# Optimization experiments

Hardware: AMD Instinct MI355X
Metric: run time of the kernel (lower is better)

## Reference

```python
import jax, jax.numpy as jnp
import numpy as np
from jax import lax

HEADS = 8
WIN_SIZES = (2, 4, 8)


def _linear(x, w, b):
    return x @ w + b


def _window_attention(x2d, ws, w4, b4):
    # x2d: (B,H,W,C); w4: (4,C,C) = [q,k,v,out]; b4: (4,C)
    B, H, W, C = x2d.shape
    p1, p2 = H // ws, W // ws
    xw = x2d.reshape(B, p1, ws, p2, ws, C).transpose(0, 1, 3, 2, 4, 5)
    xw = xw.reshape(B, p1, p2, ws * ws, C)
    hs = C // HEADS
    q = _linear(xw, w4[0], b4[0]).reshape(B, p1, p2, ws * ws, HEADS, hs)
    k = _linear(xw, w4[1], b4[1]).reshape(B, p1, p2, ws * ws, HEADS, hs)
    v = _linear(xw, w4[2], b4[2]).reshape(B, p1, p2, ws * ws, HEADS, hs)
    scores = jnp.einsum('bpqwhd,bpqvhd->bpqhwv', q, k) / jnp.sqrt(jnp.asarray(hs, x2d.dtype))
    probs = jax.nn.softmax(scores, axis=-1)
    ctx = jnp.einsum('bpqhwv,bpqvhd->bpqwhd', probs, v).reshape(B, p1, p2, ws * ws, C)
    return _linear(ctx, w4[3], b4[3])


def _unwindow(out, ws):
    B, p1, p2, win, C = out.shape
    s = out.reshape(B, p1, p2, ws, ws, C).transpose(0, 1, 3, 2, 4, 5)
    return s.reshape(B, p1 * ws, p2 * ws, C)


def _up_bilinear_ac(x, oh, ow):
    # x: (B,C,h,w); bilinear with align_corners=True (UpsamplingBilinear2d)
    B, C, h, w = x.shape
    def grid(o, i):
        pos = jnp.arange(o, dtype=x.dtype) * ((i - 1) / (o - 1))
        i0 = jnp.floor(pos).astype(jnp.int32)
        i1 = jnp.minimum(i0 + 1, i - 1)
        return i0, i1, pos - i0.astype(x.dtype)
    r0, r1, tr = grid(oh, h)
    c0, c1, tc = grid(ow, w)
    xr = x[:, :, r0, :] * (1 - tr)[None, None, :, None] + x[:, :, r1, :] * tr[None, None, :, None]
    return xr[:, :, :, c0] * (1 - tc) + xr[:, :, :, c1] * tc


def _forward(x, attn_w, attn_b, edge_w, mlp_w1, mlp_b1, mlp_w2, mlp_b2,
             dl_w, dl_b, ax_w, ax_b, g_shift, g_bias, sq_w, sq_b):
    B, N, C = x.shape
    H = W = int(np.sqrt(N))
    x2d = x.reshape(B, H, W, C)

    # multi-scale window attention branches
    scale_outputs = [_unwindow(_window_attention(x2d, ws, attn_w[i], attn_b[i]), ws)
                     for i, ws in enumerate(WIN_SIZES)]

    # adaptive window selector
    xc = x2d.transpose(0, 3, 1, 2)  # (B,C,H,W)
    edge = jnp.abs(lax.conv_general_dilated(xc, edge_w, (1, 1), 'SAME'))
    avg = lax.reduce_window(edge, 0.0, lax.add, (1, 1, 3, 3), (1, 1, 1, 1), 'SAME') / 9.0
    e = avg.transpose(0, 2, 3, 1)  # (B,H,W,1)
    wts = jax.nn.softmax(jax.nn.relu(e @ mlp_w1 + mlp_b1) @ mlp_w2 + mlp_b2, axis=-1)

    blended = sum(wts[..., i:i + 1] * scale_outputs[i] for i in range(len(WIN_SIZES)))
    h_map = blended.transpose(0, 3, 1, 2)  # (B,C,H,W)

    # ws=4 window attention -> DlightConv token pooling
    x_win = _window_attention(x2d, 4, attn_w[1], attn_b[1])  # (B,p,p,16,C)
    probs = jax.nn.softmax(jnp.mean(x_win, axis=-2) @ dl_w + dl_b, axis=-1)
    x_dl = jnp.sum(x_win * probs[..., None], axis=-2)  # (B,p,p,C)

    # axial attention (no head split, no scaling in the axial branch)
    q = _linear(x_dl, ax_w[0], ax_b[0])
    k = _linear(x_dl, ax_w[1], ax_b[1])
    v = _linear(x_dl, ax_w[2], ax_b[2])
    scores_x = jnp.einsum('bhwc,bhvc->bhwv', q, k)  # (B,r,c,k)
    scores_y = jnp.einsum('bhwc,bvwc->bwhv', q, k)  # (B,c,r,k)

    # GaussianTrans: vectorized per-pixel gaussian positional bias
    p = x_dl.shape[1]
    idx = jnp.arange(p, dtype=x.dtype)
    dist2 = (idx[None, :] - idx[:, None]) ** 2          # [pos, k]
    gb = -(g_shift[0] * dist2 + g_bias[0])              # (p,p)
    ax = jax.nn.softmax(scores_x + gb[None, None, :, :], axis=-1)       # bias indexed by c
    ay = jax.nn.softmax(jnp.swapaxes(scores_y, 1, 2) + gb[None, :, None, :], axis=-1)  # bias by r
    x_g = jnp.einsum('brck,brkd->brcd', ax, v) + jnp.einsum('brck,bkcd->brcd', ay, v)

    x_g = _up_bilinear_ac(x_g.transpose(0, 3, 1, 2), H, W)  # (B,C,H,W)

    cat = jnp.concatenate([x_g, h_map], axis=1)  # (B,2C,H,W)
    out = jnp.einsum('oc,bchw->bohw', sq_w, cat) + sq_b[None, :, None, None]
    return out.transpose(0, 2, 3, 1).reshape(B, N, C)


def setup_inputs() -> dict:
    key = jax.random.key(0)
    ks = jax.random.split(key, 16)
    B, N, C = 16, 4096, 256
    s = 0.02
    return {
        'x': jax.random.normal(ks[0], (B, N, C), jnp.float32),
        'attn_w': jax.random.normal(ks[1], (3, 4, C, C), jnp.float32) * s,
        'attn_b': jax.random.normal(ks[2], (3, 4, C), jnp.float32) * s,
        'edge_w': jax.random.normal(ks[3], (1, C, 3, 3), jnp.float32) * s,
        'mlp_w1': jax.random.normal(ks[4], (1, 16), jnp.float32) * s,
        'mlp_b1': jax.random.normal(ks[5], (16,), jnp.float32) * s,
        'mlp_w2': jax.random.normal(ks[6], (16, 3), jnp.float32) * s,
        'mlp_b2': jax.random.normal(ks[7], (3,), jnp.float32) * s,
        'dl_w': jax.random.normal(ks[8], (C, 16), jnp.float32) * s,
        'dl_b': jax.random.normal(ks[9], (16,), jnp.float32) * s,
        'ax_w': jax.random.normal(ks[10], (3, C, C), jnp.float32) * s,
        'ax_b': jax.random.normal(ks[11], (3, C), jnp.float32) * s,
        'g_shift': jnp.abs(jax.random.normal(ks[12], (1,), jnp.float32)),
        'g_bias': -jnp.abs(jax.random.normal(ks[13], (1,), jnp.float32)),
        'sq_w': jax.random.normal(ks[14], (C, 2 * C), jnp.float32) * s,
        'sq_b': jax.random.normal(ks[15], (C,), jnp.float32) * s,
    }


def reference(x, attn_w, attn_b, edge_w, mlp_w1, mlp_b1, mlp_w2, mlp_b2,
              dl_w, dl_b, ax_w, ax_b, g_shift, g_bias, sq_w, sq_b):
    return _forward(x, attn_w, attn_b, edge_w, mlp_w1, mlp_b1, mlp_w2, mlp_b2,
                    dl_w, dl_b, ax_w, ax_b, g_shift, g_bias, sq_w, sq_b)
```

## Files before the change

kernel.cpp:

```cpp
#include <hip/hip_runtime.h>
#include <math.h>


#define CHUNK_B 4
#define CHUNK_TOK (CHUNK_B * 4096)
#define KS 32

typedef __attribute__((ext_vector_type(8))) short short8;
typedef __attribute__((ext_vector_type(8))) unsigned short ushort8;
typedef __attribute__((ext_vector_type(4))) float f32x4;

__device__ __forceinline__ ushort f2bf(float f) {
    union { float f; unsigned u; } v; v.f = f;
    unsigned r = v.u + 0x7fff + ((v.u >> 16) & 1);
    return (ushort)(r >> 16);
}
__device__ __forceinline__ float bf2f(ushort h) {
    union { unsigned u; float f; } v; v.u = ((unsigned)h) << 16; return v.f;
}
__device__ __forceinline__ void split2(float v, ushort& h, ushort& l) {
    h = f2bf(v);
    l = f2bf(v - bf2f(h));
}

__device__ __forceinline__ void gld16(const ushort* g, ushort* l) {
    __builtin_amdgcn_global_load_lds(
        (const __attribute__((address_space(1))) unsigned int*)g,
        (__attribute__((address_space(3))) unsigned int*)l,
        16, 0, 0);
}

__global__ __launch_bounds__(256) void split_w_kmajor(
    const float* __restrict__ W, ushort* __restrict__ Th, ushort* __restrict__ Tl, int nmats)
{
    const int idx = blockIdx.x * 256 + threadIdx.x;
    if (idx >= nmats * 65536) return;
    const int mat = idx >> 16, r = idx & 65535;
    const int n = r >> 8, k = r & 255;
    const float v = W[(size_t)mat * 65536 + k * 256 + n];
    ushort h, l; split2(v, h, l);
    Th[idx] = h; Tl[idx] = l;
}
__global__ __launch_bounds__(256) void split_w_nmajor(
    const float* __restrict__ W, ushort* __restrict__ Th, ushort* __restrict__ Tl, int total)
{
    const int idx = blockIdx.x * 256 + threadIdx.x;
    if (idx >= total) return;
    ushort h, l; split2(W[idx], h, l);
    Th[idx] = h; Tl[idx] = l;
}

#define GEMM_DECLS                                                            \
    __shared__ ushort Ah[128 * KS], Al[128 * KS], Bh[128 * KS], Bl[128 * KS]; \
    const int tid = threadIdx.x;                                              \
    const int wave = tid >> 6, lane = tid & 63;                               \
    const int quad = lane >> 4, l16 = lane & 15;                              \
    const int wr = (wave >> 1) * 64, wc = (wave & 1) * 64;                    \
    f32x4 acc[4][4];                                                          \
    _Pragma("unroll") for (int i = 0; i < 4; i++)                             \
        _Pragma("unroll") for (int j = 0; j < 4; j++)                         \
            acc[i][j] = (f32x4){0.f, 0.f, 0.f, 0.f};                          \
    const int srow = tid >> 1;                                    \
    const int skp  = (tid & 1) * 16;

#define STAGE_GLD(dstbuf, srcp, strideE, rowbase, k0e)                        \
    _Pragma("unroll") for (int jj = 0; jj < 2; jj++) {                        \
        const int rr = (wave << 5) + (jj << 4) + (lane >> 2);                 \
        gld16((srcp) + (size_t)((rowbase) + rr) * (strideE) + (k0e) + ((lane & 3) << 3), \
              (dstbuf) + (wave << 10) + (jj << 9));                           \
    }

#define STAGE_A_SPLIT(Aptr, kk)                                               \
    {                                                                         \
        const float* srcp = (Aptr) + (size_t)(m0 + srow) * 256 + (kk) + skp;  \
        _Pragma("unroll") for (int c = 0; c < 2; c++) {                       \
            float4 v0 = *(const float4*)(srcp + c * 8);                       \
            float4 v1 = *(const float4*)(srcp + c * 8 + 4);                   \
            ushort8 h, l; ushort hh, ll;                                      \
            split2(v0.x, hh, ll); h[0] = hh; l[0] = ll;                       \
            split2(v0.y, hh, ll); h[1] = hh; l[1] = ll;                       \
            split2(v0.z, hh, ll); h[2] = hh; l[2] = ll;                       \
            split2(v0.w, hh, ll); h[3] = hh; l[3] = ll;                       \
            split2(v1.x, hh, ll); h[4] = hh; l[4] = ll;                       \
            split2(v1.y, hh, ll); h[5] = hh; l[5] = ll;                       \
            split2(v1.z, hh, ll); h[6] = hh; l[6] = ll;                       \
            split2(v1.w, hh, ll); h[7] = hh; l[7] = ll;                       \
            *(ushort8*)&Ah[srow * KS + skp + c * 8] = h;                      \
            *(ushort8*)&Al[srow * KS + skp + c * 8] = l;                      \
        }                                                                     \
    }

#define GEMM_COMPUTE                                                          \
    {                                                                         \
        short8 afh[4], afl[4], bfh[4], bfl[4];                                \
        _Pragma("unroll") for (int i = 0; i < 4; i++) {                       \
            const int ro = (wr + i * 16 + l16) * KS + quad * 8;               \
            afh[i] = *(const short8*)&Ah[ro];                                 \
            afl[i] = *(const short8*)&Al[ro];                                 \
        }                                                                     \
        _Pragma("unroll") for (int j = 0; j < 4; j++) {                       \
            const int no = (wc + j * 16 + l16) * KS + quad * 8;               \
            bfh[j] = *(const short8*)&Bh[no];                                 \
            bfl[j] = *(const short8*)&Bl[no];                                 \
        }                                                                     \
        _Pragma("unroll") for (int i = 0; i < 4; i++)                         \
            _Pragma("unroll") for (int j = 0; j < 4; j++) {                   \
                acc[i][j] = __builtin_amdgcn_mfma_f32_16x16x32_bf16(          \
                    afh[i], bfh[j], acc[i][j], 0, 0, 0);                      \
                acc[i][j] = __builtin_amdgcn_mfma_f32_16x16x32_bf16(          \
                    afl[i], bfh[j], acc[i][j], 0, 0, 0);                      \
                acc[i][j] = __builtin_amdgcn_mfma_f32_16x16x32_bf16(          \
                    afh[i], bfl[j], acc[i][j], 0, 0, 0);                      \
            }                                                                 \
    }

__global__ __launch_bounds__(256, 2) void gemm3_mfma(
    const float* __restrict__ A,
    const ushort* __restrict__ Wth, const ushort* __restrict__ Wtl,
    const float* __restrict__ b0, const float* __restrict__ b1, const float* __restrict__ b2,
    float* __restrict__ O0, float* __restrict__ O1, float* __restrict__ O2)
{
    const int m0 = blockIdx.x * 128;
    const int mat = blockIdx.y >> 1;
    const int col0 = (blockIdx.y & 1) * 128;
    const ushort* wth = Wth + (size_t)mat * 65536 + (size_t)col0 * 256;
    const ushort* wtl = Wtl + (size_t)mat * 65536 + (size_t)col0 * 256;
    GEMM_DECLS
    for (int k0 = 0; k0 < 256; k0 += 32) {
        STAGE_GLD(Bh, wth, 256, 0, k0)
        STAGE_GLD(Bl, wtl, 256, 0, k0)
        STAGE_A_SPLIT(A, k0)
        __syncthreads();
        GEMM_COMPUTE
        __syncthreads();
    }
    const float* bias = (mat == 0) ? b0 : (mat == 1) ? b1 : b2;
    float* O = (mat == 0) ? O0 : (mat == 1) ? O1 : O2;
#pragma unroll
    for (int j = 0; j < 4; j++) {
        const int col = col0 + wc + j * 16 + l16;
        const float bj = bias[col];
#pragma unroll
        for (int i = 0; i < 4; i++) {
            const int rbase = m0 + wr + i * 16 + quad * 4;
#pragma unroll
            for (int r = 0; r < 4; r++)
                O[(size_t)(rbase + r) * 256 + col] = acc[i][j][r] + bj;
        }
    }
}

__global__ __launch_bounds__(256, 2) void gemmp_mfma(
    const ushort* __restrict__ AgH, const ushort* __restrict__ AgL,
    const ushort* __restrict__ Wth, const ushort* __restrict__ Wtl,
    const float* __restrict__ bias,
    float* __restrict__ Sout, int store_s,
    float* __restrict__ Blnd, const float* __restrict__ wts, int scale_idx, int blend_init,
    int row_off)
{
    const int m0 = blockIdx.x * 128;
    const int col0 = blockIdx.y * 128;
    const ushort* wth = Wth + (size_t)col0 * 256;
    const ushort* wtl = Wtl + (size_t)col0 * 256;
    GEMM_DECLS
    (void)srow; (void)skp;
    for (int k0 = 0; k0 < 256; k0 += 32) {
        STAGE_GLD(Ah, AgH, 256, m0, k0)
        STAGE_GLD(Al, AgL, 256, m0, k0)
        STAGE_GLD(Bh, wth, 256, 0, k0)
        STAGE_GLD(Bl, wtl, 256, 0, k0)
        __syncthreads();
        GEMM_COMPUTE
        __syncthreads();
    }
#pragma unroll
    for (int i = 0; i < 4; i++) {
        const int rbase = m0 + wr + i * 16 + quad * 4;
#pragma unroll
        for (int r = 0; r < 4; r++) {
            const size_t grow = (size_t)row_off + rbase + r;
            const float wt = wts[grow * 3 + scale_idx];
#pragma unroll
            for (int j = 0; j < 4; j++) {
                const int col = col0 + wc + j * 16 + l16;
                const float v = acc[i][j][r] + bias[col];
                if (store_s) Sout[grow * 256 + col] = v;
                float* bp = Blnd + grow * 256 + col;
                if (blend_init) *bp = wt * v;
                else            *bp = *bp + wt * v;
            }
        }
    }
}

__global__ __launch_bounds__(256, 2) void gemmf_mfma(
    const ushort* __restrict__ UPH, const ushort* __restrict__ UPL,
    const float* __restrict__ BLD,
    const ushort* __restrict__ Wth, const ushort* __restrict__ Wtl,
    const float* __restrict__ SQB, float* __restrict__ OUT)
{
    const int m0 = blockIdx.x * 128;
    const int col0 = blockIdx.y * 128;
    const ushort* wth = Wth + (size_t)col0 * 512;
    const ushort* wtl = Wtl + (size_t)col0 * 512;
    GEMM_DECLS
    for (int k0 = 0; k0 < 512; k0 += 32) {
        STAGE_GLD(Bh, wth, 512, 0, k0)
        STAGE_GLD(Bl, wtl, 512, 0, k0)
        if (k0 < 256) {
            STAGE_GLD(Ah, UPH, 256, m0, k0)
            STAGE_GLD(Al, UPL, 256, m0, k0)
        } else {
            STAGE_A_SPLIT(BLD, (k0 & 255))
        }
        __syncthreads();
        GEMM_COMPUTE
        __syncthreads();
    }
#pragma unroll
    for (int j = 0; j < 4; j++) {
        const int col = col0 + wc + j * 16 + l16;
        const float bj = SQB[col];
#pragma unroll
        for (int i = 0; i < 4; i++) {
            const int rbase = m0 + wr + i * 16 + quad * 4;
#pragma unroll
            for (int r = 0; r < 4; r++)
                OUT[(size_t)(rbase + r) * 256 + col] = acc[i][j][r] + bj;
        }
    }
}

template <int WS, int NH>
__global__ __launch_bounds__(256) void win_attn(
    const float* __restrict__ Q, const float* __restrict__ K,
    const float* __restrict__ V, ushort* __restrict__ CTXh, ushort* __restrict__ CTXl)
{
    constexpr int WIN = WS * WS;
    constexpr int NW = 64 / WS;
    constexpr int CW = NH * 32;
    __shared__ float qs[WIN][CW + 4], ks[WIN][CW + 4], vs[WIN][CW + 4];
    __shared__ float sc[NH][WIN][WIN + 1];
    const int tid = threadIdx.x;
    const int wid = blockIdx.x;
    const int b = wid / (NW * NW);
    const int rem = wid % (NW * NW);
    const int p = rem / NW, q = rem % NW;
    const int h0 = blockIdx.y * NH;

    for (int idx = tid; idx < WIN * CW; idx += 256) {
        const int i = idx / CW;
        const int cc = idx % CW;
        const int ti = i / WS, tj = i % WS;
        const size_t g = ((size_t)(b * 4096 + (p * WS + ti) * 64 + (q * WS + tj))) * 256 + h0 * 32 + cc;
        qs[i][cc] = Q[g]; ks[i][cc] = K[g]; vs[i][cc] = V[g];
    }
    __syncthreads();
    const float scale = 0.17677669529663687f;
    for (int idx = tid; idx < NH * WIN * WIN; idx += 256) {
        const int hl = idx / (WIN * WIN);
        const int r = idx % (WIN * WIN);
        const int i = r / WIN, j = r % WIN;
        const int co = hl * 32;
        float s = 0.f;
#pragma unroll
        for (int d = 0; d < 32; d++) s += qs[i][co + d] * ks[j][co + d];
        sc[hl][i][j] = s * scale;
    }
    __syncthreads();
    if (tid < NH * WIN) {
        const int hl = tid / WIN, i = tid % WIN;
        float mx = -3.4e38f;
        for (int j = 0; j < WIN; j++) mx = fmaxf(mx, sc[hl][i][j]);
        float sum = 0.f;
        for (int j = 0; j < WIN; j++) {
            float e = __expf(sc[hl][i][j] - mx);
            sc[hl][i][j] = e; sum += e;
        }
        const float inv = 1.f / sum;
        for (int j = 0; j < WIN; j++) sc[hl][i][j] *= inv;
    }
    __syncthreads();
    for (int idx = tid; idx < WIN * CW; idx += 256) {
        const int i = idx / CW;
        const int cc = idx % CW;
        const int hl = cc >> 5;
        float s = 0.f;
        for (int j = 0; j < WIN; j++) s += sc[hl][i][j] * vs[j][cc];
        const int ti = i / WS, tj = i % WS;
        const size_t g = ((size_t)(b * 4096 + (p * WS + ti) * 64 + (q * WS + tj))) * 256 + h0 * 32 + cc;
        ushort hh, ll; split2(s, hh, ll);
        CTXh[g] = hh; CTXl[g] = ll;
    }
}

__global__ __launch_bounds__(256) void edge_gemm9(
    const float* __restrict__ x, const float* __restrict__ ew, float* __restrict__ ytmp)
{
    __shared__ float wsm[2304];
    const int tid = threadIdx.x;
    for (int i = tid; i < 2304; i += 256) wsm[i] = ew[i];
    __syncthreads();
    const int wave = tid >> 6, lane = tid & 63;
    const int p = blockIdx.x * 4 + wave;
    const float4 xv = *(const float4*)(x + (size_t)p * 256 + lane * 4);
    float acc[9];
#pragma unroll
    for (int t = 0; t < 9; t++) acc[t] = 0.f;
    const float xs[4] = {xv.x, xv.y, xv.z, xv.w};
#pragma unroll
    for (int i = 0; i < 4; i++) {
        const int c = lane * 4 + i;
#pragma unroll
        for (int t = 0; t < 9; t++)
            acc[t] = fmaf(xs[i], wsm[c * 9 + t], acc[t]);
    }
#pragma unroll
    for (int t = 0; t < 9; t++) {
#pragma unroll
        for (int off = 1; off < 64; off <<= 1)
            acc[t] += __shfl_xor(acc[t], off);
    }
    if (lane < 9) {
        float v = acc[0];
        switch (lane) {
            case 1: v = acc[1]; break; case 2: v = acc[2]; break;
            case 3: v = acc[3]; break; case 4: v = acc[4]; break;
            case 5: v = acc[5]; break; case 6: v = acc[6]; break;
            case 7: v = acc[7]; break; case 8: v = acc[8]; break;
            default: break;
        }
        ytmp[(size_t)p * 9 + lane] = v;
    }
}

__global__ __launch_bounds__(256) void edge_combine(
    const float* __restrict__ ytmp, float* __restrict__ edge)
{
    const int idx = blockIdx.x * 256 + threadIdx.x;
    const int b = idx >> 12, rem = idx & 4095, h = rem >> 6, w = rem & 63;
    float s = 0.f;
#pragma unroll
    for (int kh = 0; kh < 3; kh++) {
        const int hh = h + kh - 1;
        if ((unsigned)hh > 63u) continue;
#pragma unroll
        for (int kw = 0; kw < 3; kw++) {
            const int ww = w + kw - 1;
            if ((unsigned)ww > 63u) continue;
            s += ytmp[((size_t)b * 4096 + hh * 64 + ww) * 9 + kh * 3 + kw];
        }
    }
    edge[idx] = fabsf(s);
}

__global__ __launch_bounds__(256) void avg_mlp(
    const float* __restrict__ edge, const float* __restrict__ w1, const float* __restrict__ b1,
    const float* __restrict__ w2, const float* __restrict__ b2, float* __restrict__ wts)
{
    const int idx = blockIdx.x * 256 + threadIdx.x;
    const int b = idx >> 12, rem = idx & 4095, h = rem >> 6, w = rem & 63;
    float s = 0.f;
#pragma unroll
    for (int kh = -1; kh <= 1; kh++) {
        const int hh = h + kh;
        if ((unsigned)hh > 63u) continue;
#pragma unroll
        for (int kw = -1; kw <= 1; kw++) {
            const int ww = w + kw;
            if ((unsigned)ww > 63u) continue;
            s += edge[(size_t)b * 4096 + hh * 64 + ww];
        }
    }
    const float e = s / 9.f;
    float l0 = b2[0], l1 = b2[1], l2 = b2[2];
#pragma unroll
    for (int j = 0; j < 16; j++) {
        float hd = fmaxf(e * w1[j] + b1[j], 0.f);
        l0 += hd * w2[j * 3 + 0];
        l1 += hd * w2[j * 3 + 1];
        l2 += hd * w2[j * 3 + 2];
    }
    const float mx = fmaxf(l0, fmaxf(l1, l2));
    const float e0 = __expf(l0 - mx), e1 = __expf(l1 - mx), e2 = __expf(l2 - mx);
    const float inv = 1.f / (e0 + e1 + e2);
    wts[(size_t)idx * 3 + 0] = e0 * inv;
    wts[(size_t)idx * 3 + 1] = e1 * inv;
    wts[(size_t)idx * 3 + 2] = e2 * inv;
}

__global__ __launch_bounds__(256) void dlight(
    const float* __restrict__ S1, const float* __restrict__ dlw,
    const float* __restrict__ dlb, float* __restrict__ XDL)
{
    __shared__ float xw[16][257];
    __shared__ float m[256];
    __shared__ float pr[16];
    __shared__ float pr2[16];
    const int wid = blockIdx.x;
    const int b = wid >> 8, rem = wid & 255, p = rem >> 4, q = rem & 15;
    const int tid = threadIdx.x;
#pragma unroll
    for (int t = 0; t < 16; t++) {
        const int ti = t >> 2, tj = t & 3;
        xw[t][tid] = S1[((size_t)b * 4096 + (p * 4 + ti) * 64 + (q * 4 + tj)) * 256 + tid];
    }
    float mm = 0.f;
#pragma unroll
    for (int t = 0; t < 16; t++) mm += xw[t][tid];
    m[tid] = mm * (1.f / 16.f);
    __syncthreads();
    if (tid < 16) {
        float lg = dlb[tid];
        for (int c = 0; c < 256; c++) lg += m[c] * dlw[c * 16 + tid];
        pr[tid] = lg;
    }
    __syncthreads();
    if (tid < 16) {
        float mx = -3.4e38f;
        for (int j = 0; j < 16; j++) mx = fmaxf(mx, pr[j]);
        float sum = 0.f;
        for (int j = 0; j < 16; j++) sum += __expf(pr[j] - mx);
        pr2[tid] = __expf(pr[tid] - mx) / sum;
    }
    __syncthreads();
    float o = 0.f;
#pragma unroll
    for (int t = 0; t < 16; t++) o += xw[t][tid] * pr2[t];
    XDL[(size_t)wid * 256 + tid] = o;
}

__global__ __launch_bounds__(256) void axial_row(
    const float* __restrict__ Q, const float* __restrict__ K, const float* __restrict__ V,
    const float* __restrict__ gsp, const float* __restrict__ gbp, float* __restrict__ XG)
{
    __shared__ float qs[16][257], ks[16][257], vs[16][257];
    __shared__ float sc[16][17];
    const int bid = blockIdx.x;
    const int b = bid >> 4, r = bid & 15;
    const int tid = threadIdx.x;
    const float gs = gsp[0], gb = gbp[0];
#pragma unroll
    for (int w = 0; w < 16; w++) {
        const size_t base = ((size_t)b * 256 + r * 16 + w) * 256 + tid;
        qs[w][tid] = Q[base]; ks[w][tid] = K[base]; vs[w][tid] = V[base];
    }
    __syncthreads();
    {
        const int w = tid >> 4, vv = tid & 15;
        float s = 0.f;
        for (int c = 0; c < 256; c++) s += qs[w][c] * ks[vv][c];
        const float d = (float)(w - vv);
        sc[w][vv] = s - (gs * d * d + gb);
    }
    __syncthreads();
    if (tid < 16) {
        float mx = -3.4e38f;
        for (int j = 0; j < 16; j++) mx = fmaxf(mx, sc[tid][j]);
        float sum = 0.f;
        for (int j = 0; j < 16; j++) {
            float e = __expf(sc[tid][j] - mx);
            sc[tid][j] = e; sum += e;
        }
        const float inv = 1.f / sum;
        for (int j = 0; j < 16; j++) sc[tid][j] *= inv;
    }
    __syncthreads();
#pragma unroll
    for (int w2 = 0; w2 < 16; w2++) {
        float o = 0.f;
#pragma unroll
        for (int k2 = 0; k2 < 16; k2++) o += sc[w2][k2] * vs[k2][tid];
        XG[((size_t)b * 256 + r * 16 + w2) * 256 + tid] = o;
    }
}

__global__ __launch_bounds__(256) void axial_col(
    const float* __restrict__ Q, const float* __restrict__ K, const float* __restrict__ V,
    const float* __restrict__ gsp, const float* __restrict__ gbp, float* __restrict__ XG)
{
    __shared__ float qs[16][257], ks[16][257], vs[16][257];
    __shared__ float sc[16][17];
    const int bid = blockIdx.x;
    const int b = bid >> 4, col = bid & 15;
    const int tid = threadIdx.x;
    const float gs = gsp[0], gb = gbp[0];
#pragma unroll
    for (int h = 0; h < 16; h++) {
        const size_t base = ((size_t)b * 256 + h * 16 + col) * 256 + tid;
        qs[h][tid] = Q[base]; ks[h][tid] = K[base]; vs[h][tid] = V[base];
    }
    __syncthreads();
    {
        const int r = tid >> 4, vv = tid & 15;
        float s = 0.f;
        for (int c = 0; c < 256; c++) s += qs[r][c] * ks[vv][c];
        const float d = (float)(r - vv);
        sc[r][vv] = s - (gs * d * d + gb);
    }
    __syncthreads();
    if (tid < 16) {
        float mx = -3.4e38f;
        for (int j = 0; j < 16; j++) mx = fmaxf(mx, sc[tid][j]);
        float sum = 0.f;
        for (int j = 0; j < 16; j++) {
            float e = __expf(sc[tid][j] - mx);
            sc[tid][j] = e; sum += e;
        }
        const float inv = 1.f / sum;
        for (int j = 0; j < 16; j++) sc[tid][j] *= inv;
    }
    __syncthreads();
#pragma unroll
    for (int r2 = 0; r2 < 16; r2++) {
        float o = 0.f;
#pragma unroll
        for (int k2 = 0; k2 < 16; k2++) o += sc[r2][k2] * vs[k2][tid];
        XG[((size_t)b * 256 + r2 * 16 + col) * 256 + tid] += o;
    }
}

__global__ __launch_bounds__(256) void upsample(
    const float* __restrict__ XG, ushort* __restrict__ UPH, ushort* __restrict__ UPL)
{
    const unsigned idx = blockIdx.x * 256u + threadIdx.x;
    const int c = idx & 255;
    const unsigned t2 = idx >> 8;
    const int w = t2 & 63;
    const unsigned t3 = t2 >> 6;
    const int h = t3 & 63;
    const int b = t3 >> 6;
    const float rr = 15.f / 63.f;
    const float ph = h * rr, pw = w * rr;
    int h0 = (int)floorf(ph); float th = ph - (float)h0; int h1 = min(h0 + 1, 15);
    int w0 = (int)floorf(pw); float tw = pw - (float)w0; int w1 = min(w0 + 1, 15);
    const size_t bb = (size_t)b * 256;
    const float v00 = XG[((bb + h0 * 16 + w0)) * 256 + c];
    const float v10 = XG[((bb + h1 * 16 + w0)) * 256 + c];
    const float v01 = XG[((bb + h0 * 16 + w1)) * 256 + c];
    const float v11 = XG[((bb + h1 * 16 + w1)) * 256 + c];
    const float c0 = v00 * (1.f - th) + v10 * th;
    const float c1 = v01 * (1.f - th) + v11 * th;
    const float val = c0 * (1.f - tw) + c1 * tw;
    ushort hh, ll; split2(val, hh, ll);
    UPH[idx] = hh; UPL[idx] = ll;
}

extern "C" void kernel_launch(void* const* d_in, const int* in_sizes, int n_in,
                              void* d_out, int out_size, void* d_ws, size_t ws_size,
                              hipStream_t stream)
{
    const float* x      = (const float*)d_in[0];
    const float* attn_w = (const float*)d_in[1];
    const float* attn_b = (const float*)d_in[2];
    const float* edge_w = (const float*)d_in[3];
    const float* mlp_w1 = (const float*)d_in[4];
    const float* mlp_b1 = (const float*)d_in[5];
    const float* mlp_w2 = (const float*)d_in[6];
    const float* mlp_b2 = (const float*)d_in[7];
    const float* dl_w   = (const float*)d_in[8];
    const float* dl_b   = (const float*)d_in[9];
    const float* ax_w   = (const float*)d_in[10];
    const float* ax_b   = (const float*)d_in[11];
    const float* g_shift= (const float*)d_in[12];
    const float* g_bias = (const float*)d_in[13];
    const float* sq_w   = (const float*)d_in[14];
    const float* sq_b   = (const float*)d_in[15];
    float* out = (float*)d_out;

    float* ws = (float*)d_ws;
    const size_t MT = 65536;
    float* blend = ws;
    float* s1    = blend + MT * 256;
    float* scr   = s1 + MT * 256;
    float* chQ   = scr;
    float* chK   = chQ + (size_t)CHUNK_TOK * 256;
    float* chV   = chK + (size_t)CHUNK_TOK * 256;
    ushort* ctxh = (ushort*)(chV + (size_t)CHUNK_TOK * 256);
    ushort* ctxl = ctxh + (size_t)CHUNK_TOK * 256;
    ushort* uph  = (ushort*)scr;
    ushort* upl  = uph + MT * 256;
    float* ytmp  = scr;
    float* edge  = scr + MT * 256;
    float* wts   = edge + 65536;
    float* xdl   = wts + 196608;
    float* axq   = xdl + 1048576;
    float* axk   = axq + 1048576;
    float* axv   = axk + 1048576;
    float* xg    = axv + 1048576;
    ushort* Wth = (ushort*)(xg + 1048576);
    ushort* Wtl = Wth + 1114112;

    split_w_kmajor<<<(12 * 65536 + 255) / 256, 256, 0, stream>>>(attn_w, Wth, Wtl, 12);
    split_w_kmajor<<<(3 * 65536 + 255) / 256, 256, 0, stream>>>(
        ax_w, Wth + (size_t)12 * 65536, Wtl + (size_t)12 * 65536, 3);
    split_w_nmajor<<<(131072 + 255) / 256, 256, 0, stream>>>(
        sq_w, Wth + (size_t)15 * 65536, Wtl + (size_t)15 * 65536, 131072);

    edge_gemm9<<<16384, 256, 0, stream>>>(x, edge_w, ytmp);
    edge_combine<<<256, 256, 0, stream>>>(ytmp, edge);
    avg_mlp<<<256, 256, 0, stream>>>(edge, mlp_w1, mlp_b1, mlp_w2, mlp_b2, wts);

    for (int i = 0; i < 3; i++) {
        const ushort* Wh = Wth + (size_t)i * 4 * 65536;
        const ushort* Wl = Wtl + (size_t)i * 4 * 65536;
        const float* c0 = attn_b + (size_t)(i * 4 + 0) * 256;
        const float* c1 = attn_b + (size_t)(i * 4 + 1) * 256;
        const float* c2 = attn_b + (size_t)(i * 4 + 2) * 256;
        const float* c3 = attn_b + (size_t)(i * 4 + 3) * 256;
        for (int ch = 0; ch < 16 / CHUNK_B; ch++) {
            const size_t toff = (size_t)ch * CHUNK_TOK;
            const float* xc = x + toff * 256;
            gemm3_mfma<<<dim3(CHUNK_TOK / 128, 6), 256, 0, stream>>>(
                xc, Wh, Wl, c0, c1, c2, chQ, chK, chV);
            if (i == 0)
                win_attn<2, 8><<<dim3(CHUNK_B * 32 * 32, 1), 256, 0, stream>>>(chQ, chK, chV, ctxh, ctxl);
            if (i == 1)
                win_attn<4, 4><<<dim3(CHUNK_B * 16 * 16, 2), 256, 0, stream>>>(chQ, chK, chV, ctxh, ctxl);
            if (i == 2)
                win_attn<8, 1><<<dim3(CHUNK_B * 8 * 8, 8), 256, 0, stream>>>(chQ, chK, chV, ctxh, ctxl);
            gemmp_mfma<<<dim3(CHUNK_TOK / 128, 2), 256, 0, stream>>>(
                ctxh, ctxl, Wh + (size_t)3 * 65536, Wl + (size_t)3 * 65536, c3,
                s1, (i == 1) ? 1 : 0, blend, wts, i, (i == 0) ? 1 : 0, (int)toff);
        }
    }

    dlight<<<4096, 256, 0, stream>>>(s1, dl_w, dl_b, xdl);

    gemm3_mfma<<<dim3(4096 / 128, 6), 256, 0, stream>>>(
        xdl, Wth + (size_t)12 * 65536, Wtl + (size_t)12 * 65536,
        ax_b, ax_b + 256, ax_b + 512, axq, axk, axv);
    axial_row<<<256, 256, 0, stream>>>(axq, axk, axv, g_shift, g_bias, xg);
    axial_col<<<256, 256, 0, stream>>>(axq, axk, axv, g_shift, g_bias, xg);

    upsample<<<65536, 256, 0, stream>>>(xg, uph, upl);

    gemmf_mfma<<<dim3(512, 2), 256, 0, stream>>>(
        uph, upl, blend, Wth + (size_t)15 * 65536, Wtl + (size_t)15 * 65536, sq_b, out);
}
```

Measured before the change: 1.296 ms.

## Double-buffer LDS tiles in the split-bf16 MFMA GEMMs to overlap loads

```diff
diff --git a/kernel.cpp b/kernel.cpp
--- a/kernel.cpp
+++ b/kernel.cpp
@@ -51,7 +51,8 @@
 }
 
 #define GEMM_DECLS                                                            \
-    __shared__ ushort Ah[128 * KS], Al[128 * KS], Bh[128 * KS], Bl[128 * KS]; \
+    __shared__ ushort Ah[2][128 * KS], Al[2][128 * KS];                       \
+    __shared__ ushort Bh[2][128 * KS], Bl[2][128 * KS];                       \
     const int tid = threadIdx.x;                                              \
     const int wave = tid >> 6, lane = tid & 63;                               \
     const int quad = lane >> 4, l16 = lane & 15;                              \
@@ -59,9 +60,7 @@
     f32x4 acc[4][4];                                                          \
     _Pragma("unroll") for (int i = 0; i < 4; i++)                             \
         _Pragma("unroll") for (int j = 0; j < 4; j++)                         \
-            acc[i][j] = (f32x4){0.f, 0.f, 0.f, 0.f};                          \
-    const int srow = tid >> 1;                                    \
-    const int skp  = (tid & 1) * 16;
+            acc[i][j] = (f32x4){0.f, 0.f, 0.f, 0.f};
 
 #define STAGE_GLD(dstbuf, srcp, strideE, rowbase, k0e)                        \
     _Pragma("unroll") for (int jj = 0; jj < 2; jj++) {                        \
@@ -70,38 +69,44 @@
               (dstbuf) + (wave << 10) + (jj << 9));                           \
     }
 
-#define STAGE_A_SPLIT(Aptr, kk)                                               \
+#define A_LOAD(Aptr, kk)                                                      \
     {                                                                         \
-        const float* srcp = (Aptr) + (size_t)(m0 + srow) * 256 + (kk) + skp;  \
-        _Pragma("unroll") for (int c = 0; c < 2; c++) {                       \
-            float4 v0 = *(const float4*)(srcp + c * 8);                       \
-            float4 v1 = *(const float4*)(srcp + c * 8 + 4);                   \
-            ushort8 h, l; ushort hh, ll;                                      \
-            split2(v0.x, hh, ll); h[0] = hh; l[0] = ll;                       \
-            split2(v0.y, hh, ll); h[1] = hh; l[1] = ll;                       \
-            split2(v0.z, hh, ll); h[2] = hh; l[2] = ll;                       \
-            split2(v0.w, hh, ll); h[3] = hh; l[3] = ll;                       \
-            split2(v1.x, hh, ll); h[4] = hh; l[4] = ll;                       \
-            split2(v1.y, hh, ll); h[5] = hh; l[5] = ll;                       \
-            split2(v1.z, hh, ll); h[6] = hh; l[6] = ll;                       \
-            split2(v1.w, hh, ll); h[7] = hh; l[7] = ll;                       \
-            *(ushort8*)&Ah[srow * KS + skp + c * 8] = h;                      \
-            *(ushort8*)&Al[srow * KS + skp + c * 8] = l;                      \
-        }                                                                     \
-    }
-
-#define GEMM_COMPUTE                                                          \
+        const int r0 = tid >> 2, kq = (tid & 3) * 8;                          \
+        const float* p0 = (Aptr) + (size_t)(m0 + r0) * 256 + (kk) + kq;       \
+        const float* p1 = p0 + (size_t)64 * 256;                              \
+        va[0] = *(const float4*)p0; va[1] = *(const float4*)(p0 + 4);         \
+        va[2] = *(const float4*)p1; va[3] = *(const float4*)(p1 + 4);         \
+    }
+
+#define A_SPLIT_WRITE(AhD, AlD)                                               \
+    _Pragma("unroll") for (int cc = 0; cc < 2; cc++) {                        \
+        ushort8 h, l; ushort hh, ll;                                          \
+        const float4 v0 = va[cc * 2], v1 = va[cc * 2 + 1];                    \
+        split2(v0.x, hh, ll); h[0] = hh; l[0] = ll;                           \
+        split2(v0.y, hh, ll); h[1] = hh; l[1] = ll;                           \
+        split2(v0.z, hh, ll); h[2] = hh; l[2] = ll;                           \
+        split2(v0.w, hh, ll); h[3] = hh; l[3] = ll;                           \
+        split2(v1.x, hh, ll); h[4] = hh; l[4] = ll;                           \
+        split2(v1.y, hh, ll); h[5] = hh; l[5] = ll;                           \
+        split2(v1.z, hh, ll); h[6] = hh; l[6] = ll;                           \
+        split2(v1.w, hh, ll); h[7] = hh; l[7] = ll;                           \
+        const int chw = tid + cc * 256;                                       \
+        *(ushort8*)&(AhD)[chw * 8] = h;                                       \
+        *(ushort8*)&(AlD)[chw * 8] = l;                                       \
+    }
+
+#define GEMM_COMPUTE(cb)                                                      \
     {                                                                         \
         short8 afh[4], afl[4], bfh[4], bfl[4];                                \
         _Pragma("unroll") for (int i = 0; i < 4; i++) {                       \
             const int ro = (wr + i * 16 + l16) * KS + quad * 8;               \
-            afh[i] = *(const short8*)&Ah[ro];                                 \
-            afl[i] = *(const short8*)&Al[ro];                                 \
+            afh[i] = *(const short8*)&Ah[cb][ro];                             \
+            afl[i] = *(const short8*)&Al[cb][ro];                             \
         }                                                                     \
         _Pragma("unroll") for (int j = 0; j < 4; j++) {                       \
             const int no = (wc + j * 16 + l16) * KS + quad * 8;               \
-            bfh[j] = *(const short8*)&Bh[no];                                 \
-            bfl[j] = *(const short8*)&Bl[no];                                 \
+            bfh[j] = *(const short8*)&Bh[cb][no];                             \
+            bfl[j] = *(const short8*)&Bl[cb][no];                             \
         }                                                                     \
         _Pragma("unroll") for (int i = 0; i < 4; i++)                         \
             _Pragma("unroll") for (int j = 0; j < 4; j++) {                   \
@@ -126,12 +131,22 @@
     const ushort* wth = Wth + (size_t)mat * 65536 + (size_t)col0 * 256;
     const ushort* wtl = Wtl + (size_t)mat * 65536 + (size_t)col0 * 256;
     GEMM_DECLS
-    for (int k0 = 0; k0 < 256; k0 += 32) {
-        STAGE_GLD(Bh, wth, 256, 0, k0)
-        STAGE_GLD(Bl, wtl, 256, 0, k0)
-        STAGE_A_SPLIT(A, k0)
-        __syncthreads();
-        GEMM_COMPUTE
+    float4 va[4];
+    STAGE_GLD(Bh[0], wth, 256, 0, 0)
+    STAGE_GLD(Bl[0], wtl, 256, 0, 0)
+    A_LOAD(A, 0)
+    A_SPLIT_WRITE(Ah[0], Al[0])
+    __syncthreads();
+#pragma unroll
+    for (int t = 0; t < 8; ++t) {
+        const int cur = t & 1, nxt = cur ^ 1;
+        if (t < 7) {
+            STAGE_GLD(Bh[nxt], wth, 256, 0, (t + 1) * 32)
+            STAGE_GLD(Bl[nxt], wtl, 256, 0, (t + 1) * 32)
+            A_LOAD(A, (t + 1) * 32)
+        }
+        GEMM_COMPUTE(cur)
+        if (t < 7) { A_SPLIT_WRITE(Ah[nxt], Al[nxt]) }
         __syncthreads();
     }
     const float* bias = (mat == 0) ? b0 : (mat == 1) ? b1 : b2;
@@ -163,14 +178,21 @@
     const ushort* wth = Wth + (size_t)col0 * 256;
     const ushort* wtl = Wtl + (size_t)col0 * 256;
     GEMM_DECLS
-    (void)srow; (void)skp;
-    for (int k0 = 0; k0 < 256; k0 += 32) {
-        STAGE_GLD(Ah, AgH, 256, m0, k0)
-        STAGE_GLD(Al, AgL, 256, m0, k0)
-        STAGE_GLD(Bh, wth, 256, 0, k0)
-        STAGE_GLD(Bl, wtl, 256, 0, k0)
-        __syncthreads();
-        GEMM_COMPUTE
+    STAGE_GLD(Ah[0], AgH, 256, m0, 0)
+    STAGE_GLD(Al[0], AgL, 256, m0, 0)
+    STAGE_GLD(Bh[0], wth, 256, 0, 0)
+    STAGE_GLD(Bl[0], wtl, 256, 0, 0)
+    __syncthreads();
+#pragma unroll
+    for (int t = 0; t < 8; ++t) {
+        const int cur = t & 1, nxt = cur ^ 1;
+        if (t < 7) {
+            STAGE_GLD(Ah[nxt], AgH, 256, m0, (t + 1) * 32)
+            STAGE_GLD(Al[nxt], AgL, 256, m0, (t + 1) * 32)
+            STAGE_GLD(Bh[nxt], wth, 256, 0, (t + 1) * 32)
+            STAGE_GLD(Bl[nxt], wtl, 256, 0, (t + 1) * 32)
+        }
+        GEMM_COMPUTE(cur)
         __syncthreads();
     }
 #pragma unroll
@@ -204,17 +226,28 @@
     const ushort* wth = Wth + (size_t)col0 * 512;
     const ushort* wtl = Wtl + (size_t)col0 * 512;
     GEMM_DECLS
-    for (int k0 = 0; k0 < 512; k0 += 32) {
-        STAGE_GLD(Bh, wth, 512, 0, k0)
-        STAGE_GLD(Bl, wtl, 512, 0, k0)
-        if (k0 < 256) {
-            STAGE_GLD(Ah, UPH, 256, m0, k0)
-            STAGE_GLD(Al, UPL, 256, m0, k0)
-        } else {
-            STAGE_A_SPLIT(BLD, (k0 & 255))
-        }
-        __syncthreads();
-        GEMM_COMPUTE
+    float4 va[4];
+    STAGE_GLD(Bh[0], wth, 512, 0, 0)
+    STAGE_GLD(Bl[0], wtl, 512, 0, 0)
+    STAGE_GLD(Ah[0], UPH, 256, m0, 0)
+    STAGE_GLD(Al[0], UPL, 256, m0, 0)
+    __syncthreads();
+#pragma unroll
+    for (int t = 0; t < 16; ++t) {
+        const int cur = t & 1, nxt = cur ^ 1;
+        const int k1 = (t + 1) * 32;
+        if (t < 15) {
+            STAGE_GLD(Bh[nxt], wth, 512, 0, k1)
+            STAGE_GLD(Bl[nxt], wtl, 512, 0, k1)
+            if (k1 < 256) {
+                STAGE_GLD(Ah[nxt], UPH, 256, m0, k1)
+                STAGE_GLD(Al[nxt], UPL, 256, m0, k1)
+            } else {
+                A_LOAD(BLD, (k1 & 255))
+            }
+        }
+        GEMM_COMPUTE(cur)
+        if (t < 15 && k1 >= 256) { A_SPLIT_WRITE(Ah[nxt], Al[nxt]) }
         __syncthreads();
     }
 #pragma unroll
```

New measurement: 1.387 ms. 7.0% more time.

## Pre-split input to bf16 hi/lo once and stage GEMM tiles via registers

Applied to the files above, without the earlier changes.

```diff
diff --git a/kernel.cpp b/kernel.cpp
--- a/kernel.cpp
+++ b/kernel.cpp
@@ -21,13 +21,6 @@
 __device__ __forceinline__ void split2(float v, ushort& h, ushort& l) {
     h = f2bf(v);
     l = f2bf(v - bf2f(h));
-}
-
-__device__ __forceinline__ void gld16(const ushort* g, ushort* l) {
-    __builtin_amdgcn_global_load_lds(
-        (const __attribute__((address_space(1))) unsigned int*)g,
-        (__attribute__((address_space(3))) unsigned int*)l,
-        16, 0, 0);
 }
 
 __global__ __launch_bounds__(256) void split_w_kmajor(
@@ -48,6 +41,18 @@
     if (idx >= total) return;
     ushort h, l; split2(W[idx], h, l);
     Th[idx] = h; Tl[idx] = l;
+}
+
+__global__ __launch_bounds__(256) void split_x(
+    const float* __restrict__ X, ushort* __restrict__ Xh, ushort* __restrict__ Xl)
+{
+    const size_t i4 = (size_t)blockIdx.x * 256 + threadIdx.x;
+    const float4 v = *(const float4*)(X + i4 * 4);
+    ushort4 h, l;
+    split2(v.x, h.x, l.x); split2(v.y, h.y, l.y);
+    split2(v.z, h.z, l.z); split2(v.w, h.w, l.w);
+    *(ushort4*)(Xh + i4 * 4) = h;
+    *(ushort4*)(Xl + i4 * 4) = l;
 }
 
 #define GEMM_DECLS                                                            \
@@ -59,35 +64,34 @@
     f32x4 acc[4][4];                                                          \
     _Pragma("unroll") for (int i = 0; i < 4; i++)                             \
         _Pragma("unroll") for (int j = 0; j < 4; j++)                         \
-            acc[i][j] = (f32x4){0.f, 0.f, 0.f, 0.f};                          \
-    const int srow = tid >> 1;                                    \
-    const int skp  = (tid & 1) * 16;
-
-#define STAGE_GLD(dstbuf, srcp, strideE, rowbase, k0e)                        \
-    _Pragma("unroll") for (int jj = 0; jj < 2; jj++) {                        \
-        const int rr = (wave << 5) + (jj << 4) + (lane >> 2);                 \
-        gld16((srcp) + (size_t)((rowbase) + rr) * (strideE) + (k0e) + ((lane & 3) << 3), \
-              (dstbuf) + (wave << 10) + (jj << 9));                           \
-    }
-
-#define STAGE_A_SPLIT(Aptr, kk)                                               \
-    {                                                                         \
-        const float* srcp = (Aptr) + (size_t)(m0 + srow) * 256 + (kk) + skp;  \
-        _Pragma("unroll") for (int c = 0; c < 2; c++) {                       \
-            float4 v0 = *(const float4*)(srcp + c * 8);                       \
-            float4 v1 = *(const float4*)(srcp + c * 8 + 4);                   \
-            ushort8 h, l; ushort hh, ll;                                      \
-            split2(v0.x, hh, ll); h[0] = hh; l[0] = ll;                       \
-            split2(v0.y, hh, ll); h[1] = hh; l[1] = ll;                       \
-            split2(v0.z, hh, ll); h[2] = hh; l[2] = ll;                       \
-            split2(v0.w, hh, ll); h[3] = hh; l[3] = ll;                       \
-            split2(v1.x, hh, ll); h[4] = hh; l[4] = ll;                       \
-            split2(v1.y, hh, ll); h[5] = hh; l[5] = ll;                       \
-            split2(v1.z, hh, ll); h[6] = hh; l[6] = ll;                       \
-            split2(v1.w, hh, ll); h[7] = hh; l[7] = ll;                       \
-            *(ushort8*)&Ah[srow * KS + skp + c * 8] = h;                      \
-            *(ushort8*)&Al[srow * KS + skp + c * 8] = l;                      \
-        }                                                                     \
+            acc[i][j] = (f32x4){0.f, 0.f, 0.f, 0.f};
+
+#define STAGE_US(dst, src, strideE, rowbase, k0e)                             \
+    _Pragma("unroll") for (int cc = 0; cc < 2; cc++) {                        \
+        const int ch = tid + cc * 256;                                        \
+        const int r = ch >> 2, kc = (ch & 3) * 8;                             \
+        *(ushort8*)&(dst)[ch * 8] =                                           \
+            *(const ushort8*)((src) + (size_t)((rowbase) + r) * (strideE) + (k0e) + kc); \
+    }
+
+#define STAGE_F32(AhD, AlD, Aptr, kk)                                         \
+    _Pragma("unroll") for (int cc = 0; cc < 2; cc++) {                        \
+        const int ch = tid + cc * 256;                                        \
+        const int r = ch >> 2, kc = (ch & 3) * 8;                             \
+        const float* p = (Aptr) + (size_t)(m0 + r) * 256 + (kk) + kc;         \
+        const float4 v0 = *(const float4*)p;                                  \
+        const float4 v1 = *(const float4*)(p + 4);                            \
+        ushort8 h, l; ushort hh, ll;                                          \
+        split2(v0.x, hh, ll); h[0] = hh; l[0] = ll;                           \
+        split2(v0.y, hh, ll); h[1] = hh; l[1] = ll;                           \
+        split2(v0.z, hh, ll); h[2] = hh; l[2] = ll;                           \
+        split2(v0.w, hh, ll); h[3] = hh; l[3] = ll;                           \
+        split2(v1.x, hh, ll); h[4] = hh; l[4] = ll;                           \
+        split2(v1.y, hh, ll); h[5] = hh; l[5] = ll;                           \
+        split2(v1.z, hh, ll); h[6] = hh; l[6] = ll;                           \
+        split2(v1.w, hh, ll); h[7] = hh; l[7] = ll;                           \
+        *(ushort8*)&(AhD)[ch * 8] = h;                                        \
+        *(ushort8*)&(AlD)[ch * 8] = l;                                        \
     }
 
 #define GEMM_COMPUTE                                                          \
@@ -115,7 +119,7 @@
     }
 
 __global__ __launch_bounds__(256, 2) void gemm3_mfma(
-    const float* __restrict__ A,
+    const ushort* __restrict__ AgH, const ushort* __restrict__ AgL,
     const ushort* __restrict__ Wth, const ushort* __restrict__ Wtl,
     const float* __restrict__ b0, const float* __restrict__ b1, const float* __restrict__ b2,
     float* __restrict__ O0, float* __restrict__ O1, float* __restrict__ O2)
@@ -127,9 +131,10 @@
     const ushort* wtl = Wtl + (size_t)mat * 65536 + (size_t)col0 * 256;
     GEMM_DECLS
     for (int k0 = 0; k0 < 256; k0 += 32) {
-        STAGE_GLD(Bh, wth, 256, 0, k0)
-        STAGE_GLD(Bl, wtl, 256, 0, k0)
-        STAGE_A_SPLIT(A, k0)
+        STAGE_US(Ah, AgH, 256, m0, k0)
+        STAGE_US(Al, AgL, 256, m0, k0)
+        STAGE_US(Bh, wth, 256, 0, k0)
+        STAGE_US(Bl, wtl, 256, 0, k0)
         __syncthreads();
         GEMM_COMPUTE
         __syncthreads();
@@ -163,12 +168,11 @@
     const ushort* wth = Wth + (size_t)col0 * 256;
     const ushort* wtl = Wtl + (size_t)col0 * 256;
     GEMM_DECLS
-    (void)srow; (void)skp;
     for (int k0 = 0; k0 < 256; k0 += 32) {
-        STAGE_GLD(Ah, AgH, 256, m0, k0)
-        STAGE_GLD(Al, AgL, 256, m0, k0)
-        STAGE_GLD(Bh, wth, 256, 0, k0)
-        STAGE_GLD(Bl, wtl, 256, 0, k0)
+        STAGE_US(Ah, AgH, 256, m0, k0)
+        STAGE_US(Al, AgL, 256, m0, k0)
+        STAGE_US(Bh, wth, 256, 0, k0)
+        STAGE_US(Bl, wtl, 256, 0, k0)
         __syncthreads();
         GEMM_COMPUTE
         __syncthreads();
@@ -205,14 +209,14 @@
     const ushort* wtl = Wtl + (size_t)col0 * 512;
     GEMM_DECLS
     for (int k0 = 0; k0 < 512; k0 += 32) {
-        STAGE_GLD(Bh, wth, 512, 0, k0)
-        STAGE_GLD(Bl, wtl, 512, 0, k0)
         if (k0 < 256) {
-            STAGE_GLD(Ah, UPH, 256, m0, k0)
-            STAGE_GLD(Al, UPL, 256, m0, k0)
+            STAGE_US(Ah, UPH, 256, m0, k0)
+            STAGE_US(Al, UPL, 256, m0, k0)
         } else {
-            STAGE_A_SPLIT(BLD, (k0 & 255))
-        }
+            STAGE_F32(Ah, Al, BLD, (k0 & 255))
+        }
+        STAGE_US(Bh, wth, 512, 0, k0)
+        STAGE_US(Bl, wtl, 512, 0, k0)
         __syncthreads();
         GEMM_COMPUTE
         __syncthreads();
@@ -391,7 +395,7 @@
 
 __global__ __launch_bounds__(256) void dlight(
     const float* __restrict__ S1, const float* __restrict__ dlw,
-    const float* __restrict__ dlb, float* __restrict__ XDL)
+    const float* __restrict__ dlb, ushort* __restrict__ XDLH, ushort* __restrict__ XDLL)
 {
     __shared__ float xw[16][257];
     __shared__ float m[256];
@@ -427,7 +431,9 @@
     float o = 0.f;
 #pragma unroll
     for (int t = 0; t < 16; t++) o += xw[t][tid] * pr2[t];
-    XDL[(size_t)wid * 256 + tid] = o;
+    ushort hh, ll; split2(o, hh, ll);
+    XDLH[(size_t)wid * 256 + tid] = hh;
+    XDLL[(size_t)wid * 256 + tid] = ll;
 }
 
 __global__ __launch_bounds__(256) void axial_row(
@@ -584,18 +590,24 @@
     float* edge  = scr + MT * 256;
     float* wts   = edge + 65536;
     float* xdl   = wts + 196608;
+    ushort* xdlh = (ushort*)xdl;
+    ushort* xdll = xdlh + 1048576;
     float* axq   = xdl + 1048576;
     float* axk   = axq + 1048576;
     float* axv   = axk + 1048576;
     float* xg    = axv + 1048576;
     ushort* Wth = (ushort*)(xg + 1048576);
     ushort* Wtl = Wth + 1114112;
+    ushort* xh = (ushort*)out;
+    ushort* xl = xh + MT * 256;
 
     split_w_kmajor<<<(12 * 65536 + 255) / 256, 256, 0, stream>>>(attn_w, Wth, Wtl, 12);
     split_w_kmajor<<<(3 * 65536 + 255) / 256, 256, 0, stream>>>(
         ax_w, Wth + (size_t)12 * 65536, Wtl + (size_t)12 * 65536, 3);
     split_w_nmajor<<<(131072 + 255) / 256, 256, 0, stream>>>(
         sq_w, Wth + (size_t)15 * 65536, Wtl + (size_t)15 * 65536, 131072);
+
+    split_x<<<16384, 256, 0, stream>>>(x, xh, xl);
 
     edge_gemm9<<<16384, 256, 0, stream>>>(x, edge_w, ytmp);
     edge_combine<<<256, 256, 0, stream>>>(ytmp, edge);
@@ -610,9 +622,8 @@
         const float* c3 = attn_b + (size_t)(i * 4 + 3) * 256;
         for (int ch = 0; ch < 16 / CHUNK_B; ch++) {
             const size_t toff = (size_t)ch * CHUNK_TOK;
-            const float* xc = x + toff * 256;
             gemm3_mfma<<<dim3(CHUNK_TOK / 128, 6), 256, 0, stream>>>(
-                xc, Wh, Wl, c0, c1, c2, chQ, chK, chV);
+                xh + toff * 256, xl + toff * 256, Wh, Wl, c0, c1, c2, chQ, chK, chV);
             if (i == 0)
                 win_attn<2, 8><<<dim3(CHUNK_B * 32 * 32, 1), 256, 0, stream>>>(chQ, chK, chV, ctxh, ctxl);
             if (i == 1)
@@ -625,10 +636,10 @@
         }
     }
 
-    dlight<<<4096, 256, 0, stream>>>(s1, dl_w, dl_b, xdl);
+    dlight<<<4096, 256, 0, stream>>>(s1, dl_w, dl_b, xdlh, xdll);
 
     gemm3_mfma<<<dim3(4096 / 128, 6), 256, 0, stream>>>(
-        xdl, Wth + (size_t)12 * 65536, Wtl + (size_t)12 * 65536,
+        xdlh, xdll, Wth + (size_t)12 * 65536, Wtl + (size_t)12 * 65536,
         ax_b, ax_b + 256, ax_b + 512, axq, axk, axv);
     axial_row<<<256, 256, 0, stream>>>(axq, axk, axv, g_shift, g_bias, xg);
     axial_col<<<256, 256, 0, stream>>>(axq, axk, axv, g_shift, g_bias, xg);
```

Result: slower. 1.361 ms (+5.0%).
